# Kernel optimization log

Measured on AMD Instinct MI355X. Metric: run time of the kernel, lower is better.

Reference implementation:

```python
import jax, jax.numpy as jnp
import numpy as np

H = 16  # num heads
D = 64  # head dim


def rotate_half(x):
    h = x.shape[-1] // 2
    return jnp.concatenate([-x[..., h:], x[..., :h]], axis=-1)


def setup_inputs() -> dict:
    key = jax.random.key(0)
    ks = jax.random.split(key, 8)
    B, S, E = 2, 4096, 1024
    scale = 1.0 / np.sqrt(E)
    x = jax.random.normal(ks[0], (B, S, E), dtype=jnp.float32)
    Wq = jax.random.normal(ks[1], (E, E), dtype=jnp.float32) * scale
    Wk = jax.random.normal(ks[2], (E, E), dtype=jnp.float32) * scale
    Wv = jax.random.normal(ks[3], (E, E), dtype=jnp.float32) * scale
    Wg = jax.random.normal(ks[4], (E, E), dtype=jnp.float32) * scale
    Wo = jax.random.normal(ks[5], (E, E), dtype=jnp.float32) * scale
    cos = jax.random.normal(ks[6], (S, D), dtype=jnp.float32)
    sin = jax.random.normal(ks[7], (S, D), dtype=jnp.float32)
    return {"x": x, "Wq": Wq, "Wk": Wk, "Wv": Wv, "Wg": Wg, "Wo": Wo,
            "cos": cos, "sin": sin, "block_size": 256}


def reference(x, Wq, Wk, Wv, Wg, Wo, cos, sin, block_size):
    B, S, E = x.shape
    nb = S // block_size  # seq divisible by block_size (remainder==0 path)

    gate = (x @ Wg).reshape(B, S, H, D)
    q = (x @ Wq).reshape(B, S, H, D)
    k = (x @ Wk).reshape(B, S, H, D)
    v = (x @ Wv).reshape(B, S, H, D)

    # RoPE: cos/sin [S, D] -> broadcast over batch and heads (unsqueeze_dim=1 in torch
    # with [S, 1, D] after slicing gives the same broadcast over the head axis here).
    c = cos[:S][None, :, None, :]  # [1, S, 1, D]
    s = sin[:S][None, :, None, :]
    q = q * c + rotate_half(q) * s
    k = k * c + rotate_half(k) * s

    # Block-diagonal attention: reshape seq into blocks and attend within blocks only.
    def to_blocks(t):  # [B,S,H,D] -> [B,nb,H,block,D]
        return t.reshape(B, nb, block_size, H, D).transpose(0, 1, 3, 2, 4)

    qb, kb, vb = to_blocks(q), to_blocks(k), to_blocks(v)
    scores = jnp.einsum('bnhqd,bnhkd->bnhqk', qb, kb) / np.sqrt(D)
    attn = jax.nn.softmax(scores, axis=-1)
    ob = jnp.einsum('bnhqk,bnhkd->bnhqd', attn, vb)

    out = ob.transpose(0, 1, 3, 2, 4).reshape(B, S, H, D)  # back to [B,S,H,D]
    out = (out * jax.nn.sigmoid(gate)).reshape(B, S, H * D)
    return out @ Wo
```

## Files before the change

kernel.cpp:

```cpp
#include <hip/hip_runtime.h>
#include <hip/hip_bf16.h>
#include <stdint.h>

typedef __bf16 bf16_t;
typedef __bf16 bf16x8 __attribute__((ext_vector_type(8)));
typedef float f32x4 __attribute__((ext_vector_type(4)));

#define DEVI __device__ __forceinline__

constexpr int BB = 2;
constexpr int SS = 4096;
constexpr int EE = 1024;
constexpr int HH = 16;
constexpr int DD = 64;
constexpr int MM = BB * SS;

DEVI void gload16(const void* g, void* l) {
  __builtin_amdgcn_global_load_lds(
      (const __attribute__((address_space(1))) void*)g,
      (__attribute__((address_space(3))) void*)l, 16, 0, 0);
}

__global__ void cvt_kernel(const float* __restrict__ in, bf16_t* __restrict__ out, int n8) {
  int i = blockIdx.x * 256 + threadIdx.x;
  if (i >= n8) return;
  const float* p = in + (size_t)i * 8;
  bf16x8 o;
#pragma unroll
  for (int j = 0; j < 8; ++j) o[j] = (bf16_t)p[j];
  *(bf16x8*)(out + (size_t)i * 8) = o;
}

__global__ void wt_kernel(const float* __restrict__ w0, const float* __restrict__ w1,
                          const float* __restrict__ w2, const float* __restrict__ w3,
                          const float* __restrict__ w4, bf16_t* __restrict__ out) {
  __shared__ float tile[32][33];
  const float* Wsel = blockIdx.z == 0 ? w0 : blockIdx.z == 1 ? w1 :
                      blockIdx.z == 2 ? w2 : blockIdx.z == 3 ? w3 : w4;
  bf16_t* O = out + (size_t)blockIdx.z * EE * EE;
  int n0 = blockIdx.x * 32, k0 = blockIdx.y * 32;
  int tx = threadIdx.x & 31, ty = threadIdx.x >> 5;
#pragma unroll
  for (int i = 0; i < 4; ++i)
    tile[ty + i * 8][tx] = Wsel[(size_t)(k0 + ty + i * 8) * EE + n0 + tx];
  __syncthreads();
#pragma unroll
  for (int i = 0; i < 4; ++i)
    O[(size_t)(n0 + ty + i * 8) * EE + k0 + tx] = (bf16_t)tile[tx][ty + i * 8];
}

template <int MODE>
__global__ __launch_bounds__(256) void gemm_bt(const bf16_t* __restrict__ A,
                                               const bf16_t* __restrict__ Bt,
                                               void* __restrict__ Cout) {
  __shared__ bf16_t Al[128 * 64];
  __shared__ bf16_t Bl[128 * 64];
  const int m0 = blockIdx.x * 128;
  const int n0 = blockIdx.y * 128;
  const int tid = threadIdx.x;
  const int wv = tid >> 6, ln = tid & 63;
  const int wm = wv >> 1, wn = wv & 1;
  f32x4 acc[4][4] = {};

  for (int k0 = 0; k0 < EE; k0 += 64) {
    __syncthreads();
#pragma unroll
    for (int i = 0; i < 4; ++i) {
      int slot = i * 256 + wv * 64 + ln;
      int r = slot >> 3, c = slot & 7;
      int cs = c ^ (r & 7);
      gload16(A + (size_t)(m0 + r) * EE + k0 + cs * 8, Al + (size_t)(i * 256 + wv * 64) * 8);
      gload16(Bt + (size_t)(n0 + r) * EE + k0 + cs * 8, Bl + (size_t)(i * 256 + wv * 64) * 8);
    }
    __syncthreads();
#pragma unroll
    for (int kk = 0; kk < 2; ++kk) {
      bf16x8 af[4], bfr[4];
#pragma unroll
      for (int mi = 0; mi < 4; ++mi) {
        int row = wm * 64 + mi * 16 + (ln & 15);
        int ch = (kk * 4 + (ln >> 4)) ^ (row & 7);
        af[mi] = *(const bf16x8*)(Al + row * 64 + ch * 8);
      }
#pragma unroll
      for (int ni = 0; ni < 4; ++ni) {
        int row = wn * 64 + ni * 16 + (ln & 15);
        int ch = (kk * 4 + (ln >> 4)) ^ (row & 7);
        bfr[ni] = *(const bf16x8*)(Bl + row * 64 + ch * 8);
      }
#pragma unroll
      for (int mi = 0; mi < 4; ++mi)
#pragma unroll
        for (int ni = 0; ni < 4; ++ni)
          acc[mi][ni] = __builtin_amdgcn_mfma_f32_16x16x32_bf16(af[mi], bfr[ni], acc[mi][ni], 0, 0, 0);
    }
  }

  if (MODE == 0) {
    const int widx = n0 >> 10;
    const int cb = (n0 & 1023) + wn * 64;
    bf16_t* W = (bf16_t*)Cout + (size_t)widx * MM * EE;
    if (widx == 2) {
#pragma unroll
      for (int mi = 0; mi < 4; ++mi)
#pragma unroll
        for (int ni = 0; ni < 4; ++ni) {
          int row = m0 + wm * 64 + mi * 16 + ((ln >> 4) << 2);
          int ncol = cb + ni * 16 + (ln & 15);
          int h = ncol >> 6, d = ncol & 63;
          int b = row >> 12, s = row & (SS - 1);
          bf16_t* p = W + (((size_t)b * HH + h) * DD + d) * SS + s;
#pragma unroll
          for (int r = 0; r < 4; ++r) p[r] = (bf16_t)acc[mi][ni][r];
        }
    } else {
#pragma unroll
      for (int mi = 0; mi < 4; ++mi)
#pragma unroll
        for (int ni = 0; ni < 4; ++ni) {
          int row = m0 + wm * 64 + mi * 16 + ((ln >> 4) << 2);
          bf16_t* p = W + (size_t)row * EE + cb + ni * 16 + (ln & 15);
#pragma unroll
          for (int r = 0; r < 4; ++r) p[(size_t)r * EE] = (bf16_t)acc[mi][ni][r];
        }
    }
  } else {
    float* O = (float*)Cout;
#pragma unroll
    for (int mi = 0; mi < 4; ++mi)
#pragma unroll
      for (int ni = 0; ni < 4; ++ni) {
        int row = m0 + wm * 64 + mi * 16 + ((ln >> 4) << 2);
        int col = n0 + wn * 64 + ni * 16 + (ln & 15);
#pragma unroll
        for (int r = 0; r < 4; ++r) O[(size_t)(row + r) * EE + col] = acc[mi][ni][r];
      }
  }
}

__global__ __launch_bounds__(512, 4) void attn_kernel(const bf16_t* __restrict__ Q,
                                                      const bf16_t* __restrict__ Kc,
                                                      const bf16_t* __restrict__ Vt,
                                                      const bf16_t* __restrict__ G,
                                                      const float* __restrict__ cosp,
                                                      const float* __restrict__ sinp,
                                                      bf16_t* __restrict__ AO) {
  __shared__ bf16_t Kl[2][64 * 64];
  __shared__ bf16_t Vl[2][64 * 64];
  __shared__ bf16_t Pl[8][32 * 64];
  const int bx = blockIdx.x;
  const int h = bx & 15, sb = (bx >> 4) & 15, b = bx >> 8;
  const int tid = threadIdx.x, wv = tid >> 6, ln = tid & 63;
  const int qs0 = sb * 256 + wv * 32;

  bf16x8 qf[2][2];
  const int d0 = (ln >> 4) << 3;
#pragma unroll
  for (int mi = 0; mi < 2; ++mi) {
    int qs = qs0 + mi * 16 + (ln & 15);
    const bf16_t* qp = Q + ((size_t)b * SS + qs) * EE + h * DD;
    qf[mi][0] = *(const bf16x8*)(qp + d0);
    qf[mi][1] = *(const bf16x8*)(qp + 32 + d0);
    float cl[8], sl[8], chv[8], shv[8];
    *(f32x4*)&cl[0] = *(const f32x4*)&cosp[qs * DD + d0];
    *(f32x4*)&cl[4] = *(const f32x4*)&cosp[qs * DD + d0 + 4];
    *(f32x4*)&chv[0] = *(const f32x4*)&cosp[qs * DD + d0 + 32];
    *(f32x4*)&chv[4] = *(const f32x4*)&cosp[qs * DD + d0 + 36];
    *(f32x4*)&sl[0] = *(const f32x4*)&sinp[qs * DD + d0];
    *(f32x4*)&sl[4] = *(const f32x4*)&sinp[qs * DD + d0 + 4];
    *(f32x4*)&shv[0] = *(const f32x4*)&sinp[qs * DD + d0 + 32];
    *(f32x4*)&shv[4] = *(const f32x4*)&sinp[qs * DD + d0 + 36];
#pragma unroll
    for (int j = 0; j < 8; ++j) {
      float lo = (float)qf[mi][0][j], hi = (float)qf[mi][1][j];
      qf[mi][0][j] = (bf16_t)(lo * cl[j] - hi * sl[j]);
      qf[mi][1][j] = (bf16_t)(hi * chv[j] + lo * shv[j]);
    }
  }

  f32x4 o[2][4] = {};
  float mr[2][4], lr[2][4];
#pragma unroll
  for (int i = 0; i < 2; ++i)
#pragma unroll
    for (int r = 0; r < 4; ++r) { mr[i][r] = -1e30f; lr[i][r] = 0.f; }

#define STAGE_KV(KC, BI) do {                                                        \
    int r_ = tid >> 3, c_ = tid & 7, cs_ = c_ ^ (r_ & 7);                            \
    gload16(Kc + ((size_t)b * SS + sb * 256 + (KC) * 64 + r_) * EE + h * DD + cs_ * 8, \
            &Kl[BI][wv * 512]);                                                      \
    gload16(Vt + (((size_t)b * HH + h) * DD + r_) * SS + sb * 256 + (KC) * 64 + cs_ * 8, \
            &Vl[BI][wv * 512]);                                                      \
  } while (0)

  STAGE_KV(0, 0);
  __syncthreads();

  for (int kc = 0; kc < 4; ++kc) {
    const int cur = kc & 1;
    if (kc < 3) STAGE_KV(kc + 1, cur ^ 1);

    if (tid < 256) {
      int r_ = tid >> 2, c_ = tid & 3;
      int ks = sb * 256 + kc * 64 + r_;
      int chl = ((c_ ^ (r_ & 7)) << 3), chh = (((c_ ^ 4) ^ (r_ & 7)) << 3);
      bf16x8 lo8 = *(bf16x8*)&Kl[cur][r_ * 64 + chl];
      bf16x8 hi8 = *(bf16x8*)&Kl[cur][r_ * 64 + chh];
      float cl[8], sl[8], chv[8], shv[8];
      *(f32x4*)&cl[0] = *(const f32x4*)&cosp[ks * DD + c_ * 8];
      *(f32x4*)&cl[4] = *(const f32x4*)&cosp[ks * DD + c_ * 8 + 4];
      *(f32x4*)&chv[0] = *(const f32x4*)&cosp[ks * DD + c_ * 8 + 32];
      *(f32x4*)&chv[4] = *(const f32x4*)&cosp[ks * DD + c_ * 8 + 36];
      *(f32x4*)&sl[0] = *(const f32x4*)&sinp[ks * DD + c_ * 8];
      *(f32x4*)&sl[4] = *(const f32x4*)&sinp[ks * DD + c_ * 8 + 4];
      *(f32x4*)&shv[0] = *(const f32x4*)&sinp[ks * DD + c_ * 8 + 32];
      *(f32x4*)&shv[4] = *(const f32x4*)&sinp[ks * DD + c_ * 8 + 36];
      bf16x8 olo, ohi;
#pragma unroll
      for (int j = 0; j < 8; ++j) {
        float lo = (float)lo8[j], hi = (float)hi8[j];
        olo[j] = (bf16_t)(lo * cl[j] - hi * sl[j]);
        ohi[j] = (bf16_t)(hi * chv[j] + lo * shv[j]);
      }
      *(bf16x8*)&Kl[cur][r_ * 64 + chl] = olo;
      *(bf16x8*)&Kl[cur][r_ * 64 + chh] = ohi;
    }
    __syncthreads();

    f32x4 sc[2][4] = {};
    __builtin_amdgcn_s_setprio(1);
#pragma unroll
    for (int kk = 0; kk < 2; ++kk) {
      bf16x8 kf[4];
#pragma unroll
      for (int ni = 0; ni < 4; ++ni) {
        int row = ni * 16 + (ln & 15);
        int ch = (kk * 4 + (ln >> 4)) ^ (row & 7);
        kf[ni] = *(const bf16x8*)(&Kl[cur][row * 64 + ch * 8]);
      }
#pragma unroll
      for (int mi = 0; mi < 2; ++mi)
#pragma unroll
        for (int ni = 0; ni < 4; ++ni)
          sc[mi][ni] = __builtin_amdgcn_mfma_f32_16x16x32_bf16(qf[mi][kk], kf[ni], sc[mi][ni], 0, 0, 0);
    }
    __builtin_amdgcn_s_setprio(0);
#pragma unroll
    for (int mi = 0; mi < 2; ++mi)
#pragma unroll
      for (int ni = 0; ni < 4; ++ni) sc[mi][ni] *= 0.125f;

#pragma unroll
    for (int mi = 0; mi < 2; ++mi) {
#pragma unroll
      for (int r = 0; r < 4; ++r) {
        float mx = fmaxf(fmaxf(sc[mi][0][r], sc[mi][1][r]), fmaxf(sc[mi][2][r], sc[mi][3][r]));
#pragma unroll
        for (int d = 1; d < 16; d <<= 1) mx = fmaxf(mx, __shfl_xor(mx, d));
        float mn = fmaxf(mr[mi][r], mx);
        float scal = __expf(mr[mi][r] - mn);
        mr[mi][r] = mn;
        float rs = 0.f;
#pragma unroll
        for (int ni = 0; ni < 4; ++ni) {
          float p = __expf(sc[mi][ni][r] - mn);
          sc[mi][ni][r] = p;
          rs += p;
        }
#pragma unroll
        for (int d = 1; d < 16; d <<= 1) rs += __shfl_xor(rs, d);
        lr[mi][r] = lr[mi][r] * scal + rs;
#pragma unroll
        for (int nd = 0; nd < 4; ++nd) o[mi][nd][r] *= scal;
      }
    }

    bf16_t* P = Pl[wv];
#pragma unroll
    for (int mi = 0; mi < 2; ++mi)
#pragma unroll
      for (int ni = 0; ni < 4; ++ni)
#pragma unroll
        for (int r = 0; r < 4; ++r) {
          int row = mi * 16 + ((ln >> 4) << 2) + r;
          int col = ni * 16 + (ln & 15);
          P[row * 64 + (col ^ ((row & 7) << 3))] = (bf16_t)sc[mi][ni][r];
        }
    __builtin_amdgcn_s_setprio(1);
#pragma unroll
    for (int kk = 0; kk < 2; ++kk) {
      bf16x8 pf[2], vf[4];
#pragma unroll
      for (int mi = 0; mi < 2; ++mi) {
        int row = mi * 16 + (ln & 15);
        int ch = (kk * 4 + (ln >> 4)) ^ (row & 7);
        pf[mi] = *(const bf16x8*)(P + row * 64 + ch * 8);
      }
#pragma unroll
      for (int nd = 0; nd < 4; ++nd) {
        int row = nd * 16 + (ln & 15);
        int ch = (kk * 4 + (ln >> 4)) ^ (row & 7);
        vf[nd] = *(const bf16x8*)(&Vl[cur][row * 64 + ch * 8]);
      }
#pragma unroll
      for (int mi = 0; mi < 2; ++mi)
#pragma unroll
        for (int nd = 0; nd < 4; ++nd)
          o[mi][nd] = __builtin_amdgcn_mfma_f32_16x16x32_bf16(pf[mi], vf[nd], o[mi][nd], 0, 0, 0);
    }
    __builtin_amdgcn_s_setprio(0);
    __syncthreads();
  }
#undef STAGE_KV

#pragma unroll
  for (int mi = 0; mi < 2; ++mi)
#pragma unroll
    for (int r = 0; r < 4; ++r) {
      float inv = 1.f / lr[mi][r];
      int m = (int)((size_t)b * SS) + qs0 + mi * 16 + ((ln >> 4) << 2) + r;
#pragma unroll
      for (int nd = 0; nd < 4; ++nd) {
        int col = h * DD + nd * 16 + (ln & 15);
        float gv = (float)G[(size_t)m * EE + col];
        float sig = 1.f / (1.f + __expf(-gv));
        AO[(size_t)m * EE + col] = (bf16_t)((o[mi][nd][r] * inv) * sig);
      }
    }
}

extern "C" void kernel_launch(void* const* d_in, const int* in_sizes, int n_in,
                              void* d_out, int out_size, void* d_ws, size_t ws_size,
                              hipStream_t stream) {
  const float* x = (const float*)d_in[0];
  const float* Wq = (const float*)d_in[1];
  const float* Wk = (const float*)d_in[2];
  const float* Wv = (const float*)d_in[3];
  const float* Wg = (const float*)d_in[4];
  const float* Wo = (const float*)d_in[5];
  const float* cosp = (const float*)d_in[6];
  const float* sinp = (const float*)d_in[7];
  float* out = (float*)d_out;

  char* ws = (char*)d_ws;
  bf16_t* XB = (bf16_t*)(ws);
  bf16_t* WT = (bf16_t*)(ws + (16ll << 20));
  bf16_t* QB = (bf16_t*)(ws + (26ll << 20));
  bf16_t* KB = (bf16_t*)(ws + (42ll << 20));
  bf16_t* VT = (bf16_t*)(ws + (58ll << 20));
  bf16_t* GB = (bf16_t*)(ws + (74ll << 20));
  bf16_t* AO = XB;

  const int n8 = MM * EE / 8;
  cvt_kernel<<<n8 / 256, 256, 0, stream>>>(x, XB, n8);
  wt_kernel<<<dim3(32, 32, 5), 256, 0, stream>>>(Wq, Wk, Wv, Wg, Wo, WT);
  gemm_bt<0><<<dim3(MM / 128, 4 * EE / 128), 256, 0, stream>>>(XB, WT, QB);
  attn_kernel<<<BB * (SS / 256) * HH, 512, 0, stream>>>(QB, KB, VT, GB, cosp, sinp, AO);
  gemm_bt<1><<<dim3(MM / 128, EE / 128), 256, 0, stream>>>(AO, WT + (size_t)4 * EE * EE, out);
}
```

Before: 185.7 us.

## Restructure attention into full-block softmax with split query halves

The attention kernel now uses 256-thread blocks that each handle half of a 256-query block, giving twice as many blocks with a swizzled block index. The whole 256-key K and V tile is loaded into shared memory up front and RoPE is applied to K once. Softmax is then computed in a single pass over all 256 scores, which removes the online rescaling and the per-chunk barriers. In exchange each block uses more shared memory and registers (32 score accumulators per lane), and K is rotated twice per head block, once by each half. The projection GEMM's k-loop is also marked as not unrolled.

```diff
diff --git a/kernel.cpp b/kernel.cpp
--- a/kernel.cpp
+++ b/kernel.cpp
@@ -62,6 +62,7 @@
   const int wm = wv >> 1, wn = wv & 1;
   f32x4 acc[4][4] = {};
 
+#pragma unroll 1
   for (int k0 = 0; k0 < EE; k0 += 64) {
     __syncthreads();
 #pragma unroll
@@ -138,20 +139,70 @@
   }
 }
 
-__global__ __launch_bounds__(512, 4) void attn_kernel(const bf16_t* __restrict__ Q,
+__global__ __launch_bounds__(256, 2) void attn_kernel(const bf16_t* __restrict__ Q,
                                                       const bf16_t* __restrict__ Kc,
                                                       const bf16_t* __restrict__ Vt,
                                                       const bf16_t* __restrict__ G,
                                                       const float* __restrict__ cosp,
                                                       const float* __restrict__ sinp,
                                                       bf16_t* __restrict__ AO) {
-  __shared__ bf16_t Kl[2][64 * 64];
-  __shared__ bf16_t Vl[2][64 * 64];
-  __shared__ bf16_t Pl[8][32 * 64];
-  const int bx = blockIdx.x;
-  const int h = bx & 15, sb = (bx >> 4) & 15, b = bx >> 8;
+  __shared__ bf16_t Kl[256 * 64];
+  __shared__ bf16_t Vl[64 * 256];
+  __shared__ bf16_t Pl[4][32 * 64];
+  const int id = blockIdx.x;
+  const int swz = (id & 7) * 128 + (id >> 3);
+  const int half = swz & 1, ab = swz >> 1;
+  const int h = ab & 15, sb = (ab >> 4) & 15, b = ab >> 8;
   const int tid = threadIdx.x, wv = tid >> 6, ln = tid & 63;
-  const int qs0 = sb * 256 + wv * 32;
+  const int qs0 = sb * 256 + half * 128 + wv * 32;
+
+  {
+    const bf16_t* Kbase = Kc + ((size_t)b * SS + sb * 256) * EE + h * DD;
+    int kr = wv * 8 + (ln >> 3), kc8 = ln & 7;
+#pragma unroll
+    for (int g = 0; g < 8; ++g) {
+      int r = g * 32 + kr, cs = kc8 ^ (r & 7);
+      gload16(Kbase + (size_t)r * EE + cs * 8, &Kl[g * 2048 + wv * 512]);
+    }
+    const bf16_t* Vbase = Vt + ((size_t)b * HH + h) * DD * SS + sb * 256;
+    int vr = wv * 2 + (ln >> 5), vc = ln & 31;
+#pragma unroll
+    for (int g = 0; g < 8; ++g) {
+      int r = g * 8 + vr, cs = vc ^ ((r & 7) << 2);
+      gload16(Vbase + (size_t)r * SS + cs * 8, &Vl[g * 2048 + wv * 512]);
+    }
+  }
+  __syncthreads();
+
+  {
+    int c_ = tid & 3;
+#pragma unroll
+    for (int rr = 0; rr < 4; ++rr) {
+      int r_ = rr * 64 + (tid >> 2);
+      int ks = sb * 256 + r_;
+      int chl = ((c_ ^ (r_ & 7)) << 3), chh = (((c_ ^ 4) ^ (r_ & 7)) << 3);
+      bf16x8 lo8 = *(bf16x8*)&Kl[r_ * 64 + chl];
+      bf16x8 hi8 = *(bf16x8*)&Kl[r_ * 64 + chh];
+      float cl[8], sl[8], chv[8], shv[8];
+      *(f32x4*)&cl[0] = *(const f32x4*)&cosp[ks * DD + c_ * 8];
+      *(f32x4*)&cl[4] = *(const f32x4*)&cosp[ks * DD + c_ * 8 + 4];
+      *(f32x4*)&chv[0] = *(const f32x4*)&cosp[ks * DD + c_ * 8 + 32];
+      *(f32x4*)&chv[4] = *(const f32x4*)&cosp[ks * DD + c_ * 8 + 36];
+      *(f32x4*)&sl[0] = *(const f32x4*)&sinp[ks * DD + c_ * 8];
+      *(f32x4*)&sl[4] = *(const f32x4*)&sinp[ks * DD + c_ * 8 + 4];
+      *(f32x4*)&shv[0] = *(const f32x4*)&sinp[ks * DD + c_ * 8 + 32];
+      *(f32x4*)&shv[4] = *(const f32x4*)&sinp[ks * DD + c_ * 8 + 36];
+      bf16x8 olo, ohi;
+#pragma unroll
+      for (int j = 0; j < 8; ++j) {
+        float lo = (float)lo8[j], hi = (float)hi8[j];
+        olo[j] = (bf16_t)(lo * cl[j] - hi * sl[j]);
+        ohi[j] = (bf16_t)(hi * chv[j] + lo * shv[j]);
+      }
+      *(bf16x8*)&Kl[r_ * 64 + chl] = olo;
+      *(bf16x8*)&Kl[r_ * 64 + chh] = ohi;
+    }
+  }
 
   bf16x8 qf[2][2];
   const int d0 = (ln >> 4) << 3;
@@ -177,114 +228,64 @@
       qf[mi][1][j] = (bf16_t)(hi * chv[j] + lo * shv[j]);
     }
   }
+  __syncthreads();
+
+  f32x4 sc[2][16];
+#pragma unroll
+  for (int mi = 0; mi < 2; ++mi)
+#pragma unroll
+    for (int ni = 0; ni < 16; ++ni) sc[mi][ni] = f32x4{0.f, 0.f, 0.f, 0.f};
+  __builtin_amdgcn_s_setprio(1);
+#pragma unroll
+  for (int kk = 0; kk < 2; ++kk) {
+#pragma unroll
+    for (int ni = 0; ni < 16; ++ni) {
+      int row = ni * 16 + (ln & 15);
+      int ch = (kk * 4 + (ln >> 4)) ^ (row & 7);
+      bf16x8 kf = *(const bf16x8*)(&Kl[row * 64 + ch * 8]);
+#pragma unroll
+      for (int mi = 0; mi < 2; ++mi)
+        sc[mi][ni] = __builtin_amdgcn_mfma_f32_16x16x32_bf16(qf[mi][kk], kf, sc[mi][ni], 0, 0, 0);
+    }
+  }
+  __builtin_amdgcn_s_setprio(0);
+
+  float lr[2][4];
+#pragma unroll
+  for (int mi = 0; mi < 2; ++mi) {
+#pragma unroll
+    for (int r = 0; r < 4; ++r) {
+      float mx = -1e30f;
+#pragma unroll
+      for (int ni = 0; ni < 16; ++ni) mx = fmaxf(mx, sc[mi][ni][r] * 0.125f);
+#pragma unroll
+      for (int d = 1; d < 16; d <<= 1) mx = fmaxf(mx, __shfl_xor(mx, d));
+      float rs = 0.f;
+#pragma unroll
+      for (int ni = 0; ni < 16; ++ni) {
+        float p = __expf(sc[mi][ni][r] * 0.125f - mx);
+        sc[mi][ni][r] = p;
+        rs += p;
+      }
+#pragma unroll
+      for (int d = 1; d < 16; d <<= 1) rs += __shfl_xor(rs, d);
+      lr[mi][r] = rs;
+    }
+  }
 
   f32x4 o[2][4] = {};
-  float mr[2][4], lr[2][4];
-#pragma unroll
-  for (int i = 0; i < 2; ++i)
-#pragma unroll
-    for (int r = 0; r < 4; ++r) { mr[i][r] = -1e30f; lr[i][r] = 0.f; }
-
-#define STAGE_KV(KC, BI) do {                                                        \
-    int r_ = tid >> 3, c_ = tid & 7, cs_ = c_ ^ (r_ & 7);                            \
-    gload16(Kc + ((size_t)b * SS + sb * 256 + (KC) * 64 + r_) * EE + h * DD + cs_ * 8, \
-            &Kl[BI][wv * 512]);                                                      \
-    gload16(Vt + (((size_t)b * HH + h) * DD + r_) * SS + sb * 256 + (KC) * 64 + cs_ * 8, \
-            &Vl[BI][wv * 512]);                                                      \
-  } while (0)
-
-  STAGE_KV(0, 0);
-  __syncthreads();
-
+  bf16_t* P = Pl[wv];
+#pragma unroll
   for (int kc = 0; kc < 4; ++kc) {
-    const int cur = kc & 1;
-    if (kc < 3) STAGE_KV(kc + 1, cur ^ 1);
-
-    if (tid < 256) {
-      int r_ = tid >> 2, c_ = tid & 3;
-      int ks = sb * 256 + kc * 64 + r_;
-      int chl = ((c_ ^ (r_ & 7)) << 3), chh = (((c_ ^ 4) ^ (r_ & 7)) << 3);
-      bf16x8 lo8 = *(bf16x8*)&Kl[cur][r_ * 64 + chl];
-      bf16x8 hi8 = *(bf16x8*)&Kl[cur][r_ * 64 + chh];
-      float cl[8], sl[8], chv[8], shv[8];
-      *(f32x4*)&cl[0] = *(const f32x4*)&cosp[ks * DD + c_ * 8];
-      *(f32x4*)&cl[4] = *(const f32x4*)&cosp[ks * DD + c_ * 8 + 4];
-      *(f32x4*)&chv[0] = *(const f32x4*)&cosp[ks * DD + c_ * 8 + 32];
-      *(f32x4*)&chv[4] = *(const f32x4*)&cosp[ks * DD + c_ * 8 + 36];
-      *(f32x4*)&sl[0] = *(const f32x4*)&sinp[ks * DD + c_ * 8];
-      *(f32x4*)&sl[4] = *(const f32x4*)&sinp[ks * DD + c_ * 8 + 4];
-      *(f32x4*)&shv[0] = *(const f32x4*)&sinp[ks * DD + c_ * 8 + 32];
-      *(f32x4*)&shv[4] = *(const f32x4*)&sinp[ks * DD + c_ * 8 + 36];
-      bf16x8 olo, ohi;
-#pragma unroll
-      for (int j = 0; j < 8; ++j) {
-        float lo = (float)lo8[j], hi = (float)hi8[j];
-        olo[j] = (bf16_t)(lo * cl[j] - hi * sl[j]);
-        ohi[j] = (bf16_t)(hi * chv[j] + lo * shv[j]);
-      }
-      *(bf16x8*)&Kl[cur][r_ * 64 + chl] = olo;
-      *(bf16x8*)&Kl[cur][r_ * 64 + chh] = ohi;
-    }
-    __syncthreads();
-
-    f32x4 sc[2][4] = {};
-    __builtin_amdgcn_s_setprio(1);
-#pragma unroll
-    for (int kk = 0; kk < 2; ++kk) {
-      bf16x8 kf[4];
-#pragma unroll
-      for (int ni = 0; ni < 4; ++ni) {
-        int row = ni * 16 + (ln & 15);
-        int ch = (kk * 4 + (ln >> 4)) ^ (row & 7);
-        kf[ni] = *(const bf16x8*)(&Kl[cur][row * 64 + ch * 8]);
-      }
-#pragma unroll
-      for (int mi = 0; mi < 2; ++mi)
-#pragma unroll
-        for (int ni = 0; ni < 4; ++ni)
-          sc[mi][ni] = __builtin_amdgcn_mfma_f32_16x16x32_bf16(qf[mi][kk], kf[ni], sc[mi][ni], 0, 0, 0);
-    }
-    __builtin_amdgcn_s_setprio(0);
 #pragma unroll
     for (int mi = 0; mi < 2; ++mi)
 #pragma unroll
-      for (int ni = 0; ni < 4; ++ni) sc[mi][ni] *= 0.125f;
-
-#pragma unroll
-    for (int mi = 0; mi < 2; ++mi) {
-#pragma unroll
-      for (int r = 0; r < 4; ++r) {
-        float mx = fmaxf(fmaxf(sc[mi][0][r], sc[mi][1][r]), fmaxf(sc[mi][2][r], sc[mi][3][r]));
-#pragma unroll
-        for (int d = 1; d < 16; d <<= 1) mx = fmaxf(mx, __shfl_xor(mx, d));
-        float mn = fmaxf(mr[mi][r], mx);
-        float scal = __expf(mr[mi][r] - mn);
-        mr[mi][r] = mn;
-        float rs = 0.f;
-#pragma unroll
-        for (int ni = 0; ni < 4; ++ni) {
-          float p = __expf(sc[mi][ni][r] - mn);
-          sc[mi][ni][r] = p;
-          rs += p;
-        }
-#pragma unroll
-        for (int d = 1; d < 16; d <<= 1) rs += __shfl_xor(rs, d);
-        lr[mi][r] = lr[mi][r] * scal + rs;
-#pragma unroll
-        for (int nd = 0; nd < 4; ++nd) o[mi][nd][r] *= scal;
-      }
-    }
-
-    bf16_t* P = Pl[wv];
-#pragma unroll
-    for (int mi = 0; mi < 2; ++mi)
-#pragma unroll
-      for (int ni = 0; ni < 4; ++ni)
+      for (int nq = 0; nq < 4; ++nq)
 #pragma unroll
         for (int r = 0; r < 4; ++r) {
           int row = mi * 16 + ((ln >> 4) << 2) + r;
-          int col = ni * 16 + (ln & 15);
-          P[row * 64 + (col ^ ((row & 7) << 3))] = (bf16_t)sc[mi][ni][r];
+          int col = nq * 16 + (ln & 15);
+          P[row * 64 + (col ^ ((row & 7) << 3))] = (bf16_t)sc[mi][kc * 4 + nq][r];
         }
     __builtin_amdgcn_s_setprio(1);
 #pragma unroll
@@ -298,9 +299,9 @@
       }
 #pragma unroll
       for (int nd = 0; nd < 4; ++nd) {
-        int row = nd * 16 + (ln & 15);
-        int ch = (kk * 4 + (ln >> 4)) ^ (row & 7);
-        vf[nd] = *(const bf16x8*)(&Vl[cur][row * 64 + ch * 8]);
+        int d = nd * 16 + (ln & 15);
+        int c = (kc * 8 + kk * 4 + (ln >> 4)) ^ ((d & 7) << 2);
+        vf[nd] = *(const bf16x8*)(&Vl[d * 256 + c * 8]);
       }
 #pragma unroll
       for (int mi = 0; mi < 2; ++mi)
@@ -309,9 +310,7 @@
           o[mi][nd] = __builtin_amdgcn_mfma_f32_16x16x32_bf16(pf[mi], vf[nd], o[mi][nd], 0, 0, 0);
     }
     __builtin_amdgcn_s_setprio(0);
-    __syncthreads();
-  }
-#undef STAGE_KV
+  }
 
 #pragma unroll
   for (int mi = 0; mi < 2; ++mi)
@@ -355,6 +354,6 @@
   cvt_kernel<<<n8 / 256, 256, 0, stream>>>(x, XB, n8);
   wt_kernel<<<dim3(32, 32, 5), 256, 0, stream>>>(Wq, Wk, Wv, Wg, Wo, WT);
   gemm_bt<0><<<dim3(MM / 128, 4 * EE / 128), 256, 0, stream>>>(XB, WT, QB);
-  attn_kernel<<<BB * (SS / 256) * HH, 512, 0, stream>>>(QB, KB, VT, GB, cosp, sinp, AO);
+  attn_kernel<<<1024, 256, 0, stream>>>(QB, KB, VT, GB, cosp, sinp, AO);
   gemm_bt<1><<<dim3(MM / 128, EE / 128), 256, 0, stream>>>(AO, WT + (size_t)4 * EE * EE, out);
 }
```

Measured after the change: 163.8 us. 1.13x faster.
